# Kernel optimization log

Measured on AMD Instinct MI355X. Metric: run time of the kernel, lower is better.

## Reference

```python
import jax, jax.numpy as jnp
import numpy as np

N_NODES = 4096
N_HEADS = 8
NEG_SLOPE = 0.2  # PyG GATConv default leaky_relu slope


def _gat_single(h, src, dst, att_src, att_dst):
    # h: [N, H, C] projected node features; src/dst: [E] (self-loops included)
    a_s = (h * att_src).sum(-1)                      # [N, H]
    a_d = (h * att_dst).sum(-1)                      # [N, H]
    e = jax.nn.leaky_relu(a_s[src] + a_d[dst], NEG_SLOPE)   # [E, H]
    m = jax.ops.segment_max(e, dst, num_segments=N_NODES)   # [N, H]
    ex = jnp.exp(e - m[dst])                         # [E, H]
    denom = jax.ops.segment_sum(ex, dst, num_segments=N_NODES)
    alpha = ex / denom[dst]                          # [E, H] (self-loops => denom > 0)
    out = jax.ops.segment_sum(alpha[:, :, None] * h[src], dst, num_segments=N_NODES)
    return out                                       # [N, H, C]


def setup_inputs() -> dict:
    key = jax.random.key(0)
    ks = jax.random.split(key, 12)
    B, T, N, F = 4, 12, N_NODES, 8
    Hg, Hl = 64, 128
    inp = {
        "x": jax.random.normal(ks[0], (B, T, N, F), jnp.float32),
        "edge_index": jax.random.randint(ks[1], (2, 65536), 0, N, jnp.int64),
        "W_gat": jax.random.normal(ks[2], (F, Hg), jnp.float32) * 0.3,
        "att_src": jax.random.normal(ks[3], (N_HEADS, Hg // N_HEADS), jnp.float32) * 0.3,
        "att_dst": jax.random.normal(ks[4], (N_HEADS, Hg // N_HEADS), jnp.float32) * 0.3,
        "b_gat": jax.random.normal(ks[5], (Hg,), jnp.float32) * 0.1,
        "W_ih": jax.random.normal(ks[6], (4 * Hl, Hg * N), jnp.float32) * 0.002,
        "W_hh": jax.random.normal(ks[7], (4 * Hl, Hl), jnp.float32) * 0.05,
        "b_ih": jax.random.normal(ks[8], (4 * Hl,), jnp.float32) * 0.05,
        "b_hh": jax.random.normal(ks[9], (4 * Hl,), jnp.float32) * 0.05,
        "W_fc": jax.random.normal(ks[10], (Hl, N * F), jnp.float32) * 0.05,
        "b_fc": jax.random.normal(ks[11], (N * F,), jnp.float32) * 0.05,
    }
    return inp


def reference(x, edge_index, W_gat, att_src, att_dst, b_gat,
              W_ih, W_hh, b_ih, b_hh, W_fc, b_fc):
    B, T, N, F = x.shape
    H = N_HEADS
    C = W_gat.shape[1] // H
    Hl = W_hh.shape[1]

    # add self-loops (PyG GATConv default add_self_loops=True)
    loop = jnp.arange(N, dtype=edge_index.dtype)
    src = jnp.concatenate([edge_index[0], loop])
    dst = jnp.concatenate([edge_index[1], loop])

    # ---- GAT over all (batch, time) graphs at once ----
    h = (x.reshape(B * T, N, F) @ W_gat).reshape(B * T, N, H, C)
    gat = jax.vmap(_gat_single, in_axes=(0, None, None, None, None))(
        h, src, dst, att_src, att_dst)                # [BT, N, H, C]
    gat = gat.reshape(B * T, N, H * C) + b_gat
    gat = jax.nn.elu(gat)                             # dropout p=0 (eval) => identity
    seq = gat.reshape(B, T, N * H * C)

    # ---- LSTM (torch gate order: i, f, g, o) ----
    def step(carry, x_t):
        hprev, cprev = carry
        gates = x_t @ W_ih.T + b_ih + hprev @ W_hh.T + b_hh   # [B, 4Hl]
        i, f, g, o = jnp.split(gates, 4, axis=-1)
        c = jax.nn.sigmoid(f) * cprev + jax.nn.sigmoid(i) * jnp.tanh(g)
        hn = jax.nn.sigmoid(o) * jnp.tanh(c)
        return (hn, c), None

    h0 = jnp.zeros((B, Hl), x.dtype)
    (h_last, _), _ = jax.lax.scan(step, (h0, h0), seq.transpose(1, 0, 2))

    out = h_last @ W_fc + b_fc
    return out.reshape(B, N, F)
```

## Files before the change

### kernel.cpp

```cpp
#include <hip/hip_runtime.h>

#define NN 4096
#define NH 8
#define BTT 48
#define KG 262144
#define NJ 512
#define HLL 128
#define ERAW 65536
#define NKC 256
#define NG  24576

typedef __attribute__((ext_vector_type(8))) short bf16x8;
typedef __attribute__((ext_vector_type(4))) float f32x4;
typedef __attribute__((ext_vector_type(8))) unsigned short ushort8;

__device__ __forceinline__ unsigned short f2bf(float f) {
  unsigned int u = __float_as_uint(f);
  u += 0x7FFFu + ((u >> 16) & 1u);
  return (unsigned short)(u >> 16);
}
__device__ __forceinline__ float bf2f(unsigned short s) {
  return __uint_as_float(((unsigned int)s) << 16);
}

__global__ __launch_bounds__(256) void k_init(int* __restrict__ counts) {
  int t = blockIdx.x * 256 + threadIdx.x;
  counts[t] = 1;
}

__global__ __launch_bounds__(256) void k_hist(const int* __restrict__ ei, int* __restrict__ counts) {
  int e = blockIdx.x * 256 + threadIdx.x;
  atomicAdd(&counts[ei[ERAW + e]], 1);
}

__global__ __launch_bounds__(1024) void k_scan(const int* __restrict__ counts, int* __restrict__ offs,
                                               int* __restrict__ cursor, int* __restrict__ ssrc) {
  __shared__ int p[1024];
  int t = threadIdx.x;
  int i0 = t * 4;
  int c0 = counts[i0], c1 = counts[i0 + 1], c2 = counts[i0 + 2], c3 = counts[i0 + 3];
  int s = c0 + c1 + c2 + c3;
  p[t] = s;
  __syncthreads();
  for (int off = 1; off < 1024; off <<= 1) {
    int v = (t >= off) ? p[t - off] : 0;
    __syncthreads();
    p[t] += v;
    __syncthreads();
  }
  int base = p[t] - s;
  int o0 = base, o1 = o0 + c0, o2 = o1 + c1, o3 = o2 + c2;
  offs[i0] = o0; offs[i0 + 1] = o1; offs[i0 + 2] = o2; offs[i0 + 3] = o3;
  if (t == 1023) offs[NN] = o3 + c3;
  cursor[i0] = o0 + 1; cursor[i0 + 1] = o1 + 1; cursor[i0 + 2] = o2 + 1; cursor[i0 + 3] = o3 + 1;
  ssrc[o0] = i0; ssrc[o1] = i0 + 1; ssrc[o2] = i0 + 2; ssrc[o3] = i0 + 3;
}

__global__ __launch_bounds__(256) void k_scatter(const int* __restrict__ ei, int* __restrict__ cursor,
                                                 int* __restrict__ ssrc) {
  int e = blockIdx.x * 256 + threadIdx.x;
  int s = ei[e], d = ei[ERAW + e];
  int pos = atomicAdd(&cursor[d], 1);
  ssrc[pos] = s;
}

__global__ __launch_bounds__(256) void k_proj(const float* __restrict__ x, const float* __restrict__ Wg,
                                              const float* __restrict__ att_s, const float* __restrict__ att_d,
                                              unsigned short* __restrict__ h, float* __restrict__ a_s,
                                              float* __restrict__ a_d) {
  __shared__ float wgs[512];
  __shared__ float ats[64], atd[64];
  int tid = threadIdx.x;
  wgs[tid] = Wg[tid];
  wgs[256 + tid] = Wg[256 + tid];
  if (tid < 64) { ats[tid] = att_s[tid]; atd[tid] = att_d[tid]; }
  __syncthreads();
  int bt = blockIdx.x >> 7;
  int inner = blockIdx.x & 127;
  int hd = tid & 7, nl = tid >> 3;
  int n = inner * 32 + nl;
  const float* xr = x + ((size_t)(bt * NN + n)) * 8;
  float4 xa = *(const float4*)xr, xb2 = *(const float4*)(xr + 4);
  float xv[8] = {xa.x, xa.y, xa.z, xa.w, xb2.x, xb2.y, xb2.z, xb2.w};
  int hb = hd * 8;
  float hv[8];
#pragma unroll
  for (int c = 0; c < 8; ++c) {
    float acc = 0.f;
#pragma unroll
    for (int f = 0; f < 8; ++f) acc += xv[f] * wgs[f * 64 + hb + c];
    hv[c] = acc;
  }
  float as = 0.f, ad = 0.f;
#pragma unroll
  for (int c = 0; c < 8; ++c) { as += hv[c] * ats[hb + c]; ad += hv[c] * atd[hb + c]; }
  int aoff = bt * (NN * NH) + n * NH + hd;
  a_s[aoff] = as;
  a_d[aoff] = ad;
  ushort8 hr;
#pragma unroll
  for (int c = 0; c < 8; ++c) hr[c] = f2bf(hv[c]);
  *(ushort8*)(h + (size_t)bt * KG + (size_t)n * 64 + hb) = hr;
}

__global__ __launch_bounds__(256) void k_gat(const unsigned short* __restrict__ h, const float* __restrict__ a_s,
                                             const float* __restrict__ a_d, const int* __restrict__ offs,
                                             const int* __restrict__ ssrc, const float* __restrict__ b_gat,
                                             unsigned short* __restrict__ Xb) {
  int B = blockIdx.x;
  int xcd = B & 7;
  int slot = B >> 3;
  int btg = slot >> 7;
  int inner = slot & 127;
  int bt = btg * 8 + xcd;
  int tid = threadIdx.x;
  int hd = tid & 7, nl = tid >> 3;
  int n = inner * 32 + nl;
  const unsigned short* hbase = h + (size_t)bt * KG;
  const float* asb = a_s + bt * (NN * NH);
  float adn = a_d[bt * (NN * NH) + n * NH + hd];
  int beg = offs[n], end = offs[n + 1];
  float ssum = 0.f;
  float o[8];
#pragma unroll
  for (int c = 0; c < 8; ++c) o[c] = 0.f;
  for (int i = beg; i < end; ++i) {
    int s = ssrc[i];
    float e = asb[s * NH + hd] + adn;
    e = (e > 0.f) ? e : 0.2f * e;
    float p = __expf(e);
    ssum += p;
    ushort8 hvv = *(const ushort8*)(hbase + (size_t)s * 64 + hd * 8);
#pragma unroll
    for (int c = 0; c < 8; ++c) o[c] += p * bf2f(hvv[c]);
  }
  float inv = 1.f / ssum;
  ushort8 r;
#pragma unroll
  for (int c = 0; c < 8; ++c) {
    float v = o[c] * inv + b_gat[hd * 8 + c];
    v = (v > 0.f) ? v : (__expf(v) - 1.f);
    r[c] = f2bf(v);
  }
  *(ushort8*)(Xb + (size_t)bt * KG + (size_t)n * 64 + hd * 8) = r;
}

__global__ __launch_bounds__(256) void k_gemm(const unsigned short* __restrict__ Xb,
                                              const float* __restrict__ Wih, float* __restrict__ Gp) {
  int tid = threadIdx.x;
  int w = tid >> 6, lane = tid & 63;
  int lm = lane & 15, kg = lane >> 4;
  int b = blockIdx.x;
  int xcd = b & 7;
  int q = b >> 3;
  int kc = xcd * 32 + (q >> 2);
  int jb = q & 3;
  int j0 = jb * 128 + w * 32;
  size_t kbase = (size_t)kc * 1024 + kg * 8;

  const float* wr0 = Wih + (size_t)(j0 + lm) * KG + kbase;
  const float* wr1 = Wih + (size_t)(j0 + 16 + lm) * KG + kbase;
  const short* Xs = (const short*)Xb;
  const short* xr0 = Xs + (size_t)lm * KG + kbase;
  const short* xr1 = xr0 + (size_t)16 * KG;
  const short* xr2 = xr0 + (size_t)32 * KG;

  f32x4 acc[3][2];
#pragma unroll
  for (int mf = 0; mf < 3; ++mf)
#pragma unroll
    for (int jf = 0; jf < 2; ++jf) acc[mf][jf] = f32x4{0.f, 0.f, 0.f, 0.f};

  float4 wbuf[2][4];
  bf16x8 abuf[2][3];

  wbuf[0][0] = *(const float4*)(wr0);
  wbuf[0][1] = *(const float4*)(wr0 + 4);
  wbuf[0][2] = *(const float4*)(wr1);
  wbuf[0][3] = *(const float4*)(wr1 + 4);
  abuf[0][0] = *(const bf16x8*)(xr0);
  abuf[0][1] = *(const bf16x8*)(xr1);
  abuf[0][2] = *(const bf16x8*)(xr2);

#pragma unroll 2
  for (int t = 0; t < 32; ++t) {
    int cur = t & 1, nxt = cur ^ 1;
    if (t + 1 < 32) {
      int off = (t + 1) * 32;
      wbuf[nxt][0] = *(const float4*)(wr0 + off);
      wbuf[nxt][1] = *(const float4*)(wr0 + off + 4);
      wbuf[nxt][2] = *(const float4*)(wr1 + off);
      wbuf[nxt][3] = *(const float4*)(wr1 + off + 4);
      abuf[nxt][0] = *(const bf16x8*)(xr0 + off);
      abuf[nxt][1] = *(const bf16x8*)(xr1 + off);
      abuf[nxt][2] = *(const bf16x8*)(xr2 + off);
    }
#pragma unroll
    for (int jf = 0; jf < 2; ++jf) {
      float4 f0 = wbuf[cur][jf * 2], f1 = wbuf[cur][jf * 2 + 1];
      bf16x8 bb;
      bb[0] = (short)f2bf(f0.x); bb[1] = (short)f2bf(f0.y);
      bb[2] = (short)f2bf(f0.z); bb[3] = (short)f2bf(f0.w);
      bb[4] = (short)f2bf(f1.x); bb[5] = (short)f2bf(f1.y);
      bb[6] = (short)f2bf(f1.z); bb[7] = (short)f2bf(f1.w);
      acc[0][jf] = __builtin_amdgcn_mfma_f32_16x16x32_bf16(abuf[cur][0], bb, acc[0][jf], 0, 0, 0);
      acc[1][jf] = __builtin_amdgcn_mfma_f32_16x16x32_bf16(abuf[cur][1], bb, acc[1][jf], 0, 0, 0);
      acc[2][jf] = __builtin_amdgcn_mfma_f32_16x16x32_bf16(abuf[cur][2], bb, acc[2][jf], 0, 0, 0);
    }
  }

  float* gout = Gp + (size_t)kc * NG;
#pragma unroll
  for (int mf = 0; mf < 3; ++mf)
#pragma unroll
    for (int jf = 0; jf < 2; ++jf) {
      int j = j0 + jf * 16 + lm;
#pragma unroll
      for (int r = 0; r < 4; ++r) {
        int bt = mf * 16 + kg * 4 + r;
        gout[bt * NJ + j] = acc[mf][jf][r];
      }
    }
}

__global__ __launch_bounds__(256) void k_red1(const float* __restrict__ Gp, float* __restrict__ Gp2) {
  int idx = blockIdx.x * 256 + threadIdx.x;
  int seg = idx / NG;
  int gid = idx - seg * NG;
  const float* src = Gp + (size_t)seg * 32 * NG + gid;
  float acc = 0.f;
#pragma unroll 8
  for (int i = 0; i < 32; ++i) acc += src[(size_t)i * NG];
  Gp2[idx] = acc;
}

__global__ __launch_bounds__(512) void k_lstm(const float* __restrict__ Gp2, const float* __restrict__ Whh,
                                              const float* __restrict__ bih, const float* __restrict__ bhh,
                                              float* __restrict__ hlast) {
  __shared__ float hs[HLL];
  __shared__ float gs[NJ];
  int b = blockIdx.x, j = threadIdx.x;
  float bias = bih[j] + bhh[j];
  float w[HLL];
  const float* wr = Whh + (size_t)j * HLL;
#pragma unroll
  for (int k = 0; k < HLL; k += 4) {
    float4 v = *(const float4*)(wr + k);
    w[k] = v.x; w[k + 1] = v.y; w[k + 2] = v.z; w[k + 3] = v.w;
  }
  if (j < HLL) hs[j] = 0.f;
  float c = 0.f;
  __syncthreads();
  for (int t = 0; t < 12; ++t) {
    const float* gp = Gp2 + (size_t)(b * 12 + t) * NJ + j;
    float acc = bias;
#pragma unroll
    for (int s = 0; s < 8; ++s) acc += gp[(size_t)s * NG];
#pragma unroll
    for (int k = 0; k < HLL; ++k) acc += w[k] * hs[k];
    gs[j] = acc;
    __syncthreads();
    if (j < HLL) {
      float gi = gs[j], gf = gs[HLL + j], gg = gs[2 * HLL + j], go = gs[3 * HLL + j];
      float si = 1.f / (1.f + __expf(-gi));
      float sf = 1.f / (1.f + __expf(-gf));
      float so = 1.f / (1.f + __expf(-go));
      c = sf * c + si * tanhf(gg);
      hs[j] = so * tanhf(c);
    }
    __syncthreads();
  }
  if (j < HLL) hlast[b * HLL + j] = hs[j];
}

__global__ __launch_bounds__(256) void k_fc(const float* __restrict__ hlast, const float* __restrict__ Wfc,
                                            const float* __restrict__ bfc, float* __restrict__ out) {
  __shared__ float hl[NJ];
  int tid = threadIdx.x;
  hl[tid] = hlast[tid];
  hl[256 + tid] = hlast[256 + tid];
  __syncthreads();
  int n = blockIdx.x * 256 + tid;
  float a0 = 0.f, a1 = 0.f, a2 = 0.f, a3 = 0.f;
#pragma unroll 8
  for (int k = 0; k < HLL; ++k) {
    float wv = Wfc[(size_t)k * 32768 + n];
    a0 += hl[k] * wv;
    a1 += hl[HLL + k] * wv;
    a2 += hl[2 * HLL + k] * wv;
    a3 += hl[3 * HLL + k] * wv;
  }
  float bb = bfc[n];
  out[n] = a0 + bb;
  out[32768 + n] = a1 + bb;
  out[65536 + n] = a2 + bb;
  out[98304 + n] = a3 + bb;
}

extern "C" void kernel_launch(void* const* d_in, const int* in_sizes, int n_in,
                              void* d_out, int out_size, void* d_ws, size_t ws_size,
                              hipStream_t stream) {
  const float* x     = (const float*)d_in[0];
  const int*   ei    = (const int*)d_in[1];
  const float* Wg    = (const float*)d_in[2];
  const float* att_s = (const float*)d_in[3];
  const float* att_d = (const float*)d_in[4];
  const float* b_gat = (const float*)d_in[5];
  const float* Wih   = (const float*)d_in[6];
  const float* Whh   = (const float*)d_in[7];
  const float* bih   = (const float*)d_in[8];
  const float* bhh   = (const float*)d_in[9];
  const float* Wfc   = (const float*)d_in[10];
  const float* bfc   = (const float*)d_in[11];
  float* out = (float*)d_out;

  char* ws = (char*)d_ws;
  unsigned short* h  = (unsigned short*)(ws);
  float* a_s         = (float*)(ws + 25165824);
  float* a_d         = (float*)(ws + 31457280);
  unsigned short* Xb = (unsigned short*)(ws + 37748736);
  float* Gp          = (float*)(ws + 62914560);
  float* Gp2         = (float*)(ws + 88080384);
  float* hlast       = (float*)(ws + 88866816);
  int* counts        = (int*)(ws + 88868864);
  int* offs          = (int*)(ws + 88885248);
  int* cursor        = (int*)(ws + 88901644);
  int* ssrc          = (int*)(ws + 88918028);

  hipLaunchKernelGGL(k_init,    dim3(16),       dim3(256),  0, stream, counts);
  hipLaunchKernelGGL(k_hist,    dim3(256),      dim3(256),  0, stream, ei, counts);
  hipLaunchKernelGGL(k_scan,    dim3(1),        dim3(1024), 0, stream, counts, offs, cursor, ssrc);
  hipLaunchKernelGGL(k_scatter, dim3(256),      dim3(256),  0, stream, ei, cursor, ssrc);
  hipLaunchKernelGGL(k_proj,    dim3(48 * 128), dim3(256),  0, stream, x, Wg, att_s, att_d, h, a_s, a_d);
  hipLaunchKernelGGL(k_gat,     dim3(48 * 128), dim3(256),  0, stream, h, a_s, a_d, offs, ssrc, b_gat, Xb);
  hipLaunchKernelGGL(k_gemm,    dim3(1024),     dim3(256),  0, stream, Xb, Wih, Gp);
  hipLaunchKernelGGL(k_red1,    dim3(768),      dim3(256),  0, stream, Gp, Gp2);
  hipLaunchKernelGGL(k_lstm,    dim3(4),        dim3(512),  0, stream, Gp2, Whh, bih, bhh, hlast);
  hipLaunchKernelGGL(k_fc,      dim3(128),      dim3(256),  0, stream, hlast, Wfc, bfc, out);
}
```

Measured before the change: 320.1 us.

## Fuse whole pipeline into one cooperative persistent kernel with grid syncs

Replaces the ten separate launches with a single cooperative kernel of 512 blocks that runs the stages (histogram plus projection, scan, scatter, GAT, GEMM, reduction, LSTM, FC) separated by grid.sync. The GAT stage now processes two batch-time slices per edge walk, so the CSR index loads are shared across slices. The goal is to remove launch gaps and inter-kernel drain, at the cost of grid-barrier overhead and a fixed, smaller grid that may underfill stages such as the GEMM. The old multi-kernel path is kept as a fallback if the cooperative launch fails.

```diff
diff --git a/kernel.cpp b/kernel.cpp
--- a/kernel.cpp
+++ b/kernel.cpp
@@ -1,4 +1,7 @@
 #include <hip/hip_runtime.h>
+#include <hip/hip_cooperative_groups.h>
+
+namespace cg = cooperative_groups;
 
 #define NN 4096
 #define NH 8
@@ -23,16 +26,309 @@
   return __uint_as_float(((unsigned int)s) << 16);
 }
 
+__global__ __launch_bounds__(256, 2) void k_mega(
+    const float* __restrict__ x, const int* __restrict__ ei, const float* __restrict__ Wg,
+    const float* __restrict__ att_s, const float* __restrict__ att_d, const float* __restrict__ b_gat,
+    const float* __restrict__ Wih, const float* __restrict__ Whh, const float* __restrict__ bih,
+    const float* __restrict__ bhh, const float* __restrict__ Wfc, const float* __restrict__ bfc,
+    float* __restrict__ out, unsigned short* __restrict__ h, float* __restrict__ a_s,
+    float* __restrict__ a_d, unsigned short* __restrict__ Xb, float* __restrict__ Gp,
+    float* __restrict__ Gp2, float* __restrict__ hlast, int* __restrict__ counts,
+    int* __restrict__ offs, int* __restrict__ cursor, int* __restrict__ ssrc) {
+  cg::grid_group grid = cg::this_grid();
+  __shared__ float smem[768];
+  const int tid = threadIdx.x;
+  const int bid = blockIdx.x;
+  const int gid = bid * 256 + tid;
+
+  if (gid < ERAW) atomicAdd(&counts[ei[ERAW + gid]], 1);
+  smem[tid] = Wg[tid];
+  smem[256 + tid] = Wg[256 + tid];
+  if (tid < 64) { smem[512 + tid] = att_s[tid]; smem[576 + tid] = att_d[tid]; }
+  __syncthreads();
+  {
+    int hd = tid & 7, nl = tid >> 3, hb = hd * 8;
+    for (int iter = 0; iter < 12; ++iter) {
+      int vb = iter * 512 + bid;
+      int bt = vb >> 7, inner = vb & 127;
+      int n = inner * 32 + nl;
+      const float* xr = x + ((size_t)(bt * NN + n)) * 8;
+      float4 xa = *(const float4*)xr, xb2 = *(const float4*)(xr + 4);
+      float xv[8] = {xa.x, xa.y, xa.z, xa.w, xb2.x, xb2.y, xb2.z, xb2.w};
+      float hv[8];
+#pragma unroll
+      for (int c = 0; c < 8; ++c) {
+        float acc = 0.f;
+#pragma unroll
+        for (int f = 0; f < 8; ++f) acc += xv[f] * smem[f * 64 + hb + c];
+        hv[c] = acc;
+      }
+      float as = 0.f, ad = 0.f;
+#pragma unroll
+      for (int c = 0; c < 8; ++c) { as += hv[c] * smem[512 + hb + c]; ad += hv[c] * smem[576 + hb + c]; }
+      int aoff = bt * (NN * NH) + n * NH + hd;
+      a_s[aoff] = as;
+      a_d[aoff] = ad;
+      ushort8 hr;
+#pragma unroll
+      for (int c = 0; c < 8; ++c) hr[c] = f2bf(hv[c]);
+      *(ushort8*)(h + (size_t)bt * KG + (size_t)n * 64 + hb) = hr;
+    }
+  }
+  __threadfence();
+  grid.sync();
+
+  if (bid == 0) {
+    int* ip = (int*)smem;
+    int i0 = tid * 16;
+    int c[16];
+    int s = 0;
+#pragma unroll
+    for (int k = 0; k < 16; ++k) { c[k] = counts[i0 + k] + 1; s += c[k]; }
+    ip[tid] = s;
+    __syncthreads();
+    for (int off = 1; off < 256; off <<= 1) {
+      int v = (tid >= off) ? ip[tid - off] : 0;
+      __syncthreads();
+      ip[tid] += v;
+      __syncthreads();
+    }
+    int run = ip[tid] - s;
+#pragma unroll
+    for (int k = 0; k < 16; ++k) {
+      offs[i0 + k] = run;
+      cursor[i0 + k] = run + 1;
+      ssrc[run] = i0 + k;
+      run += c[k];
+    }
+    if (tid == 255) offs[NN] = run;
+  }
+  __threadfence();
+  grid.sync();
+
+  if (gid < ERAW) {
+    int s2 = ei[gid], d = ei[ERAW + gid];
+    int pos = atomicAdd(&cursor[d], 1);
+    ssrc[pos] = s2;
+  }
+  __threadfence();
+  grid.sync();
+
+  {
+    int hd = tid & 7, nl = tid >> 3, hb = hd * 8;
+    int xcd = bid & 7, q = bid >> 3;
+    float bg[8];
+#pragma unroll
+    for (int c = 0; c < 8; ++c) bg[c] = b_gat[hb + c];
+    for (int half = 0; half < 2; ++half) {
+      int n = (half * 64 + q) * 32 + nl;
+      int beg = offs[n], end = offs[n + 1];
+      for (int pr = 0; pr < 3; ++pr) {
+        int bt0 = (2 * pr) * 8 + xcd;
+        int bt1 = (2 * pr + 1) * 8 + xcd;
+        const unsigned short* hb0 = h + (size_t)bt0 * KG;
+        const unsigned short* hb1 = h + (size_t)bt1 * KG;
+        const float* as0 = a_s + bt0 * (NN * NH);
+        const float* as1 = a_s + bt1 * (NN * NH);
+        float ad0 = a_d[bt0 * (NN * NH) + n * NH + hd];
+        float ad1 = a_d[bt1 * (NN * NH) + n * NH + hd];
+        float ss0 = 0.f, ss1 = 0.f;
+        float o0[8], o1[8];
+#pragma unroll
+        for (int c = 0; c < 8; ++c) { o0[c] = 0.f; o1[c] = 0.f; }
+        for (int i = beg; i < end; ++i) {
+          int s = ssrc[i];
+          float e0 = as0[s * NH + hd] + ad0;
+          float e1 = as1[s * NH + hd] + ad1;
+          e0 = (e0 > 0.f) ? e0 : 0.2f * e0;
+          e1 = (e1 > 0.f) ? e1 : 0.2f * e1;
+          float p0 = __expf(e0), p1 = __expf(e1);
+          ss0 += p0; ss1 += p1;
+          ushort8 v0 = *(const ushort8*)(hb0 + (size_t)s * 64 + hb);
+          ushort8 v1 = *(const ushort8*)(hb1 + (size_t)s * 64 + hb);
+#pragma unroll
+          for (int c = 0; c < 8; ++c) { o0[c] += p0 * bf2f(v0[c]); o1[c] += p1 * bf2f(v1[c]); }
+        }
+        float i0 = 1.f / ss0, i1 = 1.f / ss1;
+        ushort8 r0, r1;
+#pragma unroll
+        for (int c = 0; c < 8; ++c) {
+          float u0 = o0[c] * i0 + bg[c];
+          float u1 = o1[c] * i1 + bg[c];
+          u0 = (u0 > 0.f) ? u0 : (__expf(u0) - 1.f);
+          u1 = (u1 > 0.f) ? u1 : (__expf(u1) - 1.f);
+          r0[c] = f2bf(u0); r1[c] = f2bf(u1);
+        }
+        *(ushort8*)(Xb + (size_t)bt0 * KG + (size_t)n * 64 + hb) = r0;
+        *(ushort8*)(Xb + (size_t)bt1 * KG + (size_t)n * 64 + hb) = r1;
+      }
+    }
+  }
+  __threadfence();
+  grid.sync();
+
+  {
+    int w = tid >> 6, lane = tid & 63;
+    int lm = lane & 15, kg = lane >> 4;
+    const short* Xs = (const short*)Xb;
+    for (int it = 0; it < 2; ++it) {
+      int vb = it * 512 + bid;
+      int jb = vb & 3;
+      int kc = vb >> 2;
+      int j0 = jb * 128 + w * 32;
+      size_t kbase = (size_t)kc * 1024 + kg * 8;
+
+      const float* wr0 = Wih + (size_t)(j0 + lm) * KG + kbase;
+      const float* wr1 = Wih + (size_t)(j0 + 16 + lm) * KG + kbase;
+      const short* xr0 = Xs + (size_t)lm * KG + kbase;
+      const short* xr1 = xr0 + (size_t)16 * KG;
+      const short* xr2 = xr0 + (size_t)32 * KG;
+
+      f32x4 acc[3][2];
+#pragma unroll
+      for (int mf = 0; mf < 3; ++mf)
+#pragma unroll
+        for (int jf = 0; jf < 2; ++jf) acc[mf][jf] = f32x4{0.f, 0.f, 0.f, 0.f};
+
+      float4 wbuf[2][4];
+      bf16x8 abuf[2][3];
+      wbuf[0][0] = *(const float4*)(wr0);
+      wbuf[0][1] = *(const float4*)(wr0 + 4);
+      wbuf[0][2] = *(const float4*)(wr1);
+      wbuf[0][3] = *(const float4*)(wr1 + 4);
+      abuf[0][0] = *(const bf16x8*)(xr0);
+      abuf[0][1] = *(const bf16x8*)(xr1);
+      abuf[0][2] = *(const bf16x8*)(xr2);
+
+#pragma unroll 2
+      for (int t = 0; t < 32; ++t) {
+        int cur = t & 1, nxt = cur ^ 1;
+        if (t + 1 < 32) {
+          int off = (t + 1) * 32;
+          wbuf[nxt][0] = *(const float4*)(wr0 + off);
+          wbuf[nxt][1] = *(const float4*)(wr0 + off + 4);
+          wbuf[nxt][2] = *(const float4*)(wr1 + off);
+          wbuf[nxt][3] = *(const float4*)(wr1 + off + 4);
+          abuf[nxt][0] = *(const bf16x8*)(xr0 + off);
+          abuf[nxt][1] = *(const bf16x8*)(xr1 + off);
+          abuf[nxt][2] = *(const bf16x8*)(xr2 + off);
+        }
+#pragma unroll
+        for (int jf = 0; jf < 2; ++jf) {
+          float4 f0 = wbuf[cur][jf * 2], f1 = wbuf[cur][jf * 2 + 1];
+          bf16x8 bb;
+          bb[0] = (short)f2bf(f0.x); bb[1] = (short)f2bf(f0.y);
+          bb[2] = (short)f2bf(f0.z); bb[3] = (short)f2bf(f0.w);
+          bb[4] = (short)f2bf(f1.x); bb[5] = (short)f2bf(f1.y);
+          bb[6] = (short)f2bf(f1.z); bb[7] = (short)f2bf(f1.w);
+          acc[0][jf] = __builtin_amdgcn_mfma_f32_16x16x32_bf16(abuf[cur][0], bb, acc[0][jf], 0, 0, 0);
+          acc[1][jf] = __builtin_amdgcn_mfma_f32_16x16x32_bf16(abuf[cur][1], bb, acc[1][jf], 0, 0, 0);
+          acc[2][jf] = __builtin_amdgcn_mfma_f32_16x16x32_bf16(abuf[cur][2], bb, acc[2][jf], 0, 0, 0);
+        }
+      }
+
+      float* gout = Gp + (size_t)kc * NG;
+#pragma unroll
+      for (int mf = 0; mf < 3; ++mf)
+#pragma unroll
+        for (int jf = 0; jf < 2; ++jf) {
+          int j = j0 + jf * 16 + lm;
+#pragma unroll
+          for (int r = 0; r < 4; ++r) {
+            int bt = mf * 16 + kg * 4 + r;
+            gout[bt * NJ + j] = acc[mf][jf][r];
+          }
+        }
+    }
+  }
+  __threadfence();
+  grid.sync();
+
+  for (int idx = gid; idx < 8 * NG; idx += 512 * 256) {
+    int seg = idx / NG;
+    int g2 = idx - seg * NG;
+    const float* src = Gp + (size_t)seg * 32 * NG + g2;
+    float acc = 0.f;
+#pragma unroll 8
+    for (int i = 0; i < 32; ++i) acc += src[(size_t)i * NG];
+    Gp2[idx] = acc;
+  }
+  __threadfence();
+  grid.sync();
+
+  if (bid < 4) {
+    float* hs = smem;
+    float* gs = smem + 128;
+    int b = bid;
+    int j0 = tid, j1 = tid + 256;
+    float bias0 = bih[j0] + bhh[j0];
+    float bias1 = bih[j1] + bhh[j1];
+    if (tid < 128) hs[tid] = 0.f;
+    float cc = 0.f;
+    __syncthreads();
+    const float4* w0 = (const float4*)(Whh + (size_t)j0 * HLL);
+    const float4* w1 = (const float4*)(Whh + (size_t)j1 * HLL);
+    for (int t = 0; t < 12; ++t) {
+      const float* gp = Gp2 + (size_t)(b * 12 + t) * NJ;
+      float acc0 = bias0, acc1 = bias1;
+#pragma unroll
+      for (int s = 0; s < 8; ++s) { acc0 += gp[s * NG + j0]; acc1 += gp[s * NG + j1]; }
+#pragma unroll 8
+      for (int k = 0; k < 32; ++k) {
+        float4 wa = w0[k], wb = w1[k];
+        int kb = k * 4;
+        acc0 += wa.x * hs[kb] + wa.y * hs[kb + 1] + wa.z * hs[kb + 2] + wa.w * hs[kb + 3];
+        acc1 += wb.x * hs[kb] + wb.y * hs[kb + 1] + wb.z * hs[kb + 2] + wb.w * hs[kb + 3];
+      }
+      gs[j0] = acc0;
+      gs[j1] = acc1;
+      __syncthreads();
+      if (tid < 128) {
+        float gi = gs[tid], gf = gs[128 + tid], gg = gs[256 + tid], go = gs[384 + tid];
+        float si = 1.f / (1.f + __expf(-gi));
+        float sf = 1.f / (1.f + __expf(-gf));
+        float so = 1.f / (1.f + __expf(-go));
+        cc = sf * cc + si * tanhf(gg);
+        hs[tid] = so * tanhf(cc);
+      }
+      __syncthreads();
+    }
+    if (tid < 128) hlast[b * HLL + tid] = hs[tid];
+  }
+  __threadfence();
+  grid.sync();
+
+  if (bid < 128) {
+    float* hl = smem;
+    hl[tid] = hlast[tid];
+    hl[256 + tid] = hlast[256 + tid];
+    __syncthreads();
+    int n = bid * 256 + tid;
+    float a0 = 0.f, a1 = 0.f, a2 = 0.f, a3 = 0.f;
+#pragma unroll 8
+    for (int k = 0; k < HLL; ++k) {
+      float wv = Wfc[(size_t)k * 32768 + n];
+      a0 += hl[k] * wv;
+      a1 += hl[HLL + k] * wv;
+      a2 += hl[2 * HLL + k] * wv;
+      a3 += hl[3 * HLL + k] * wv;
+    }
+    float bb = bfc[n];
+    out[n] = a0 + bb;
+    out[32768 + n] = a1 + bb;
+    out[65536 + n] = a2 + bb;
+    out[98304 + n] = a3 + bb;
+  }
+}
+
 __global__ __launch_bounds__(256) void k_init(int* __restrict__ counts) {
   int t = blockIdx.x * 256 + threadIdx.x;
   counts[t] = 1;
 }
-
 __global__ __launch_bounds__(256) void k_hist(const int* __restrict__ ei, int* __restrict__ counts) {
   int e = blockIdx.x * 256 + threadIdx.x;
   atomicAdd(&counts[ei[ERAW + e]], 1);
 }
-
 __global__ __launch_bounds__(1024) void k_scan(const int* __restrict__ counts, int* __restrict__ offs,
                                                int* __restrict__ cursor, int* __restrict__ ssrc) {
   __shared__ int p[1024];
@@ -55,7 +351,6 @@
   cursor[i0] = o0 + 1; cursor[i0 + 1] = o1 + 1; cursor[i0 + 2] = o2 + 1; cursor[i0 + 3] = o3 + 1;
   ssrc[o0] = i0; ssrc[o1] = i0 + 1; ssrc[o2] = i0 + 2; ssrc[o3] = i0 + 3;
 }
-
 __global__ __launch_bounds__(256) void k_scatter(const int* __restrict__ ei, int* __restrict__ cursor,
                                                  int* __restrict__ ssrc) {
   int e = blockIdx.x * 256 + threadIdx.x;
@@ -63,7 +358,6 @@
   int pos = atomicAdd(&cursor[d], 1);
   ssrc[pos] = s;
 }
-
 __global__ __launch_bounds__(256) void k_proj(const float* __restrict__ x, const float* __restrict__ Wg,
                                               const float* __restrict__ att_s, const float* __restrict__ att_d,
                                               unsigned short* __restrict__ h, float* __restrict__ a_s,
@@ -102,7 +396,6 @@
   for (int c = 0; c < 8; ++c) hr[c] = f2bf(hv[c]);
   *(ushort8*)(h + (size_t)bt * KG + (size_t)n * 64 + hb) = hr;
 }
-
 __global__ __launch_bounds__(256) void k_gat(const unsigned short* __restrict__ h, const float* __restrict__ a_s,
                                              const float* __restrict__ a_d, const int* __restrict__ offs,
                                              const int* __restrict__ ssrc, const float* __restrict__ b_gat,
@@ -144,36 +437,28 @@
   }
   *(ushort8*)(Xb + (size_t)bt * KG + (size_t)n * 64 + hd * 8) = r;
 }
-
 __global__ __launch_bounds__(256) void k_gemm(const unsigned short* __restrict__ Xb,
                                               const float* __restrict__ Wih, float* __restrict__ Gp) {
   int tid = threadIdx.x;
   int w = tid >> 6, lane = tid & 63;
   int lm = lane & 15, kg = lane >> 4;
-  int b = blockIdx.x;
-  int xcd = b & 7;
-  int q = b >> 3;
-  int kc = xcd * 32 + (q >> 2);
-  int jb = q & 3;
+  int jb = blockIdx.x & 3;
+  int kc = blockIdx.x >> 2;
   int j0 = jb * 128 + w * 32;
   size_t kbase = (size_t)kc * 1024 + kg * 8;
-
   const float* wr0 = Wih + (size_t)(j0 + lm) * KG + kbase;
   const float* wr1 = Wih + (size_t)(j0 + 16 + lm) * KG + kbase;
   const short* Xs = (const short*)Xb;
   const short* xr0 = Xs + (size_t)lm * KG + kbase;
   const short* xr1 = xr0 + (size_t)16 * KG;
   const short* xr2 = xr0 + (size_t)32 * KG;
-
   f32x4 acc[3][2];
 #pragma unroll
   for (int mf = 0; mf < 3; ++mf)
 #pragma unroll
     for (int jf = 0; jf < 2; ++jf) acc[mf][jf] = f32x4{0.f, 0.f, 0.f, 0.f};
-
   float4 wbuf[2][4];
   bf16x8 abuf[2][3];
-
   wbuf[0][0] = *(const float4*)(wr0);
   wbuf[0][1] = *(const float4*)(wr0 + 4);
   wbuf[0][2] = *(const float4*)(wr1);
@@ -181,7 +466,6 @@
   abuf[0][0] = *(const bf16x8*)(xr0);
   abuf[0][1] = *(const bf16x8*)(xr1);
   abuf[0][2] = *(const bf16x8*)(xr2);
-
 #pragma unroll 2
   for (int t = 0; t < 32; ++t) {
     int cur = t & 1, nxt = cur ^ 1;
@@ -208,7 +492,6 @@
       acc[2][jf] = __builtin_amdgcn_mfma_f32_16x16x32_bf16(abuf[cur][2], bb, acc[2][jf], 0, 0, 0);
     }
   }
-
   float* gout = Gp + (size_t)kc * NG;
 #pragma unroll
   for (int mf = 0; mf < 3; ++mf)
@@ -222,7 +505,6 @@
       }
     }
 }
-
 __global__ __launch_bounds__(256) void k_red1(const float* __restrict__ Gp, float* __restrict__ Gp2) {
   int idx = blockIdx.x * 256 + threadIdx.x;
   int seg = idx / NG;
@@ -233,7 +515,6 @@
   for (int i = 0; i < 32; ++i) acc += src[(size_t)i * NG];
   Gp2[idx] = acc;
 }
-
 __global__ __launch_bounds__(512) void k_lstm(const float* __restrict__ Gp2, const float* __restrict__ Whh,
                                               const float* __restrict__ bih, const float* __restrict__ bhh,
                                               float* __restrict__ hlast) {
@@ -272,7 +553,6 @@
   }
   if (j < HLL) hlast[b * HLL + j] = hs[j];
 }
-
 __global__ __launch_bounds__(256) void k_fc(const float* __restrict__ hlast, const float* __restrict__ Wfc,
                                             const float* __restrict__ bfc, float* __restrict__ out) {
   __shared__ float hl[NJ];
@@ -324,17 +604,28 @@
   float* hlast       = (float*)(ws + 88866816);
   int* counts        = (int*)(ws + 88868864);
   int* offs          = (int*)(ws + 88885248);
-  int* cursor        = (int*)(ws + 88901644);
-  int* ssrc          = (int*)(ws + 88918028);
-
-  hipLaunchKernelGGL(k_init,    dim3(16),       dim3(256),  0, stream, counts);
-  hipLaunchKernelGGL(k_hist,    dim3(256),      dim3(256),  0, stream, ei, counts);
-  hipLaunchKernelGGL(k_scan,    dim3(1),        dim3(1024), 0, stream, counts, offs, cursor, ssrc);
-  hipLaunchKernelGGL(k_scatter, dim3(256),      dim3(256),  0, stream, ei, cursor, ssrc);
-  hipLaunchKernelGGL(k_proj,    dim3(48 * 128), dim3(256),  0, stream, x, Wg, att_s, att_d, h, a_s, a_d);
-  hipLaunchKernelGGL(k_gat,     dim3(48 * 128), dim3(256),  0, stream, h, a_s, a_d, offs, ssrc, b_gat, Xb);
-  hipLaunchKernelGGL(k_gemm,    dim3(1024),     dim3(256),  0, stream, Xb, Wih, Gp);
-  hipLaunchKernelGGL(k_red1,    dim3(768),      dim3(256),  0, stream, Gp, Gp2);
-  hipLaunchKernelGGL(k_lstm,    dim3(4),        dim3(512),  0, stream, Gp2, Whh, bih, bhh, hlast);
-  hipLaunchKernelGGL(k_fc,      dim3(128),      dim3(256),  0, stream, hlast, Wfc, bfc, out);
-}
+  int* cursor        = (int*)(ws + 88901648);
+  int* ssrc          = (int*)(ws + 88918032);
+
+  hipMemsetAsync(counts, 0, NN * sizeof(int), stream);
+
+  void* args[] = {
+      (void*)&x, (void*)&ei, (void*)&Wg, (void*)&att_s, (void*)&att_d, (void*)&b_gat,
+      (void*)&Wih, (void*)&Whh, (void*)&bih, (void*)&bhh, (void*)&Wfc, (void*)&bfc,
+      (void*)&out, (void*)&h, (void*)&a_s, (void*)&a_d, (void*)&Xb, (void*)&Gp,
+      (void*)&Gp2, (void*)&hlast, (void*)&counts, (void*)&offs, (void*)&cursor, (void*)&ssrc};
+  hipError_t err = hipLaunchCooperativeKernel((void*)k_mega, dim3(512), dim3(256), args, 0, stream);
+
+  if (err != hipSuccess) {
+    hipLaunchKernelGGL(k_init,    dim3(16),       dim3(256),  0, stream, counts);
+    hipLaunchKernelGGL(k_hist,    dim3(256),      dim3(256),  0, stream, ei, counts);
+    hipLaunchKernelGGL(k_scan,    dim3(1),        dim3(1024), 0, stream, counts, offs, cursor, ssrc);
+    hipLaunchKernelGGL(k_scatter, dim3(256),      dim3(256),  0, stream, ei, cursor, ssrc);
+    hipLaunchKernelGGL(k_proj,    dim3(48 * 128), dim3(256),  0, stream, x, Wg, att_s, att_d, h, a_s, a_d);
+    hipLaunchKernelGGL(k_gat,     dim3(48 * 128), dim3(256),  0, stream, h, a_s, a_d, offs, ssrc, b_gat, Xb);
+    hipLaunchKernelGGL(k_gemm,    dim3(1024),     dim3(256),  0, stream, Xb, Wih, Gp);
+    hipLaunchKernelGGL(k_red1,    dim3(768),      dim3(256),  0, stream, Gp, Gp2);
+    hipLaunchKernelGGL(k_lstm,    dim3(4),        dim3(512),  0, stream, Gp2, Whh, bih, bhh, hlast);
+    hipLaunchKernelGGL(k_fc,      dim3(128),      dim3(256),  0, stream, hlast, Wfc, bfc, out);
+  }
+}
```

New measurement: 1.089 ms. 3.4x slower.

## Replace CSR build with fixed-capacity per-node buckets, add nontemporal weight loads

Applied to the files above, without the earlier changes.

Removes the count, histogram and single-block scan kernels. Edges and self-loops are now scattered directly into fixed 64-slot buckets per destination node, with the atomic cursor serving as the degree. The GEMM streams W_ih with nontemporal loads and drops the XCD-aware block remapping. The bucket scheme assumes in-degree never exceeds 64, which is a data-dependent risk: random edges give a mean in-degree of about 17, so overflow is unlikely but not ruled out.

```diff
diff --git a/kernel.cpp b/kernel.cpp
--- a/kernel.cpp
+++ b/kernel.cpp
@@ -9,6 +9,7 @@
 #define ERAW 65536
 #define NKC 256
 #define NG  24576
+#define CAP 64
 
 typedef __attribute__((ext_vector_type(8))) short bf16x8;
 typedef __attribute__((ext_vector_type(4))) float f32x4;
@@ -22,46 +23,23 @@
 __device__ __forceinline__ float bf2f(unsigned short s) {
   return __uint_as_float(((unsigned int)s) << 16);
 }
-
-__global__ __launch_bounds__(256) void k_init(int* __restrict__ counts) {
-  int t = blockIdx.x * 256 + threadIdx.x;
-  counts[t] = 1;
-}
-
-__global__ __launch_bounds__(256) void k_hist(const int* __restrict__ ei, int* __restrict__ counts) {
-  int e = blockIdx.x * 256 + threadIdx.x;
-  atomicAdd(&counts[ei[ERAW + e]], 1);
-}
-
-__global__ __launch_bounds__(1024) void k_scan(const int* __restrict__ counts, int* __restrict__ offs,
-                                               int* __restrict__ cursor, int* __restrict__ ssrc) {
-  __shared__ int p[1024];
-  int t = threadIdx.x;
-  int i0 = t * 4;
-  int c0 = counts[i0], c1 = counts[i0 + 1], c2 = counts[i0 + 2], c3 = counts[i0 + 3];
-  int s = c0 + c1 + c2 + c3;
-  p[t] = s;
-  __syncthreads();
-  for (int off = 1; off < 1024; off <<= 1) {
-    int v = (t >= off) ? p[t - off] : 0;
-    __syncthreads();
-    p[t] += v;
-    __syncthreads();
-  }
-  int base = p[t] - s;
-  int o0 = base, o1 = o0 + c0, o2 = o1 + c1, o3 = o2 + c2;
-  offs[i0] = o0; offs[i0 + 1] = o1; offs[i0 + 2] = o2; offs[i0 + 3] = o3;
-  if (t == 1023) offs[NN] = o3 + c3;
-  cursor[i0] = o0 + 1; cursor[i0 + 1] = o1 + 1; cursor[i0 + 2] = o2 + 1; cursor[i0 + 3] = o3 + 1;
-  ssrc[o0] = i0; ssrc[o1] = i0 + 1; ssrc[o2] = i0 + 2; ssrc[o3] = i0 + 3;
+__device__ __forceinline__ float4 nt_load4(const float* p) {
+  f32x4 v = __builtin_nontemporal_load((const f32x4*)p);
+  return float4{v[0], v[1], v[2], v[3]};
 }
 
 __global__ __launch_bounds__(256) void k_scatter(const int* __restrict__ ei, int* __restrict__ cursor,
                                                  int* __restrict__ ssrc) {
-  int e = blockIdx.x * 256 + threadIdx.x;
-  int s = ei[e], d = ei[ERAW + e];
-  int pos = atomicAdd(&cursor[d], 1);
-  ssrc[pos] = s;
+  int t = blockIdx.x * 256 + threadIdx.x;
+  if (t < ERAW) {
+    int s = ei[t], d = ei[ERAW + t];
+    int pos = atomicAdd(&cursor[d], 1);
+    ssrc[(d << 6) + pos] = s;
+  } else {
+    int n = t - ERAW;
+    int pos = atomicAdd(&cursor[n], 1);
+    ssrc[(n << 6) + pos] = n;
+  }
 }
 
 __global__ __launch_bounds__(256) void k_proj(const float* __restrict__ x, const float* __restrict__ Wg,
@@ -104,7 +82,7 @@
 }
 
 __global__ __launch_bounds__(256) void k_gat(const unsigned short* __restrict__ h, const float* __restrict__ a_s,
-                                             const float* __restrict__ a_d, const int* __restrict__ offs,
+                                             const float* __restrict__ a_d, const int* __restrict__ cursor,
                                              const int* __restrict__ ssrc, const float* __restrict__ b_gat,
                                              unsigned short* __restrict__ Xb) {
   int B = blockIdx.x;
@@ -119,13 +97,14 @@
   const unsigned short* hbase = h + (size_t)bt * KG;
   const float* asb = a_s + bt * (NN * NH);
   float adn = a_d[bt * (NN * NH) + n * NH + hd];
-  int beg = offs[n], end = offs[n + 1];
+  int deg = cursor[n];
+  const int* bucket = ssrc + (n << 6);
   float ssum = 0.f;
   float o[8];
 #pragma unroll
   for (int c = 0; c < 8; ++c) o[c] = 0.f;
-  for (int i = beg; i < end; ++i) {
-    int s = ssrc[i];
+  for (int i = 0; i < deg; ++i) {
+    int s = bucket[i];
     float e = asb[s * NH + hd] + adn;
     e = (e > 0.f) ? e : 0.2f * e;
     float p = __expf(e);
@@ -150,11 +129,8 @@
   int tid = threadIdx.x;
   int w = tid >> 6, lane = tid & 63;
   int lm = lane & 15, kg = lane >> 4;
-  int b = blockIdx.x;
-  int xcd = b & 7;
-  int q = b >> 3;
-  int kc = xcd * 32 + (q >> 2);
-  int jb = q & 3;
+  int jb = blockIdx.x & 3;
+  int kc = blockIdx.x >> 2;
   int j0 = jb * 128 + w * 32;
   size_t kbase = (size_t)kc * 1024 + kg * 8;
 
@@ -174,10 +150,10 @@
   float4 wbuf[2][4];
   bf16x8 abuf[2][3];
 
-  wbuf[0][0] = *(const float4*)(wr0);
-  wbuf[0][1] = *(const float4*)(wr0 + 4);
-  wbuf[0][2] = *(const float4*)(wr1);
-  wbuf[0][3] = *(const float4*)(wr1 + 4);
+  wbuf[0][0] = nt_load4(wr0);
+  wbuf[0][1] = nt_load4(wr0 + 4);
+  wbuf[0][2] = nt_load4(wr1);
+  wbuf[0][3] = nt_load4(wr1 + 4);
   abuf[0][0] = *(const bf16x8*)(xr0);
   abuf[0][1] = *(const bf16x8*)(xr1);
   abuf[0][2] = *(const bf16x8*)(xr2);
@@ -187,10 +163,10 @@
     int cur = t & 1, nxt = cur ^ 1;
     if (t + 1 < 32) {
       int off = (t + 1) * 32;
-      wbuf[nxt][0] = *(const float4*)(wr0 + off);
-      wbuf[nxt][1] = *(const float4*)(wr0 + off + 4);
-      wbuf[nxt][2] = *(const float4*)(wr1 + off);
-      wbuf[nxt][3] = *(const float4*)(wr1 + off + 4);
+      wbuf[nxt][0] = nt_load4(wr0 + off);
+      wbuf[nxt][1] = nt_load4(wr0 + off + 4);
+      wbuf[nxt][2] = nt_load4(wr1 + off);
+      wbuf[nxt][3] = nt_load4(wr1 + off + 4);
       abuf[nxt][0] = *(const bf16x8*)(xr0 + off);
       abuf[nxt][1] = *(const bf16x8*)(xr1 + off);
       abuf[nxt][2] = *(const bf16x8*)(xr2 + off);
@@ -320,21 +296,17 @@
   float* a_d         = (float*)(ws + 31457280);
   unsigned short* Xb = (unsigned short*)(ws + 37748736);
   float* Gp          = (float*)(ws + 62914560);
+  int* ssrc          = (int*)(ws + 87031808);
   float* Gp2         = (float*)(ws + 88080384);
   float* hlast       = (float*)(ws + 88866816);
-  int* counts        = (int*)(ws + 88868864);
-  int* offs          = (int*)(ws + 88885248);
-  int* cursor        = (int*)(ws + 88901644);
-  int* ssrc          = (int*)(ws + 88918028);
-
-  hipLaunchKernelGGL(k_init,    dim3(16),       dim3(256),  0, stream, counts);
-  hipLaunchKernelGGL(k_hist,    dim3(256),      dim3(256),  0, stream, ei, counts);
-  hipLaunchKernelGGL(k_scan,    dim3(1),        dim3(1024), 0, stream, counts, offs, cursor, ssrc);
-  hipLaunchKernelGGL(k_scatter, dim3(256),      dim3(256),  0, stream, ei, cursor, ssrc);
-  hipLaunchKernelGGL(k_proj,    dim3(48 * 128), dim3(256),  0, stream, x, Wg, att_s, att_d, h, a_s, a_d);
-  hipLaunchKernelGGL(k_gat,     dim3(48 * 128), dim3(256),  0, stream, h, a_s, a_d, offs, ssrc, b_gat, Xb);
-  hipLaunchKernelGGL(k_gemm,    dim3(1024),     dim3(256),  0, stream, Xb, Wih, Gp);
-  hipLaunchKernelGGL(k_red1,    dim3(768),      dim3(256),  0, stream, Gp, Gp2);
-  hipLaunchKernelGGL(k_lstm,    dim3(4),        dim3(512),  0, stream, Gp2, Whh, bih, bhh, hlast);
-  hipLaunchKernelGGL(k_fc,      dim3(128),      dim3(256),  0, stream, hlast, Wfc, bfc, out);
-}
+  int* cursor        = (int*)(ws + 88868864);
+
+  hipMemsetAsync(cursor, 0, NN * sizeof(int), stream);
+  hipLaunchKernelGGL(k_scatter, dim3(272),      dim3(256), 0, stream, ei, cursor, ssrc);
+  hipLaunchKernelGGL(k_proj,    dim3(48 * 128), dim3(256), 0, stream, x, Wg, att_s, att_d, h, a_s, a_d);
+  hipLaunchKernelGGL(k_gat,     dim3(48 * 128), dim3(256), 0, stream, h, a_s, a_d, cursor, ssrc, b_gat, Xb);
+  hipLaunchKernelGGL(k_gemm,    dim3(1024),     dim3(256), 0, stream, Xb, Wih, Gp);
+  hipLaunchKernelGGL(k_red1,    dim3(768),      dim3(256), 0, stream, Gp, Gp2);
+  hipLaunchKernelGGL(k_lstm,    dim3(4),        dim3(512), 0, stream, Gp2, Whh, bih, bhh, hlast);
+  hipLaunchKernelGGL(k_fc,      dim3(128),      dim3(256), 0, stream, hlast, Wfc, bfc, out);
+}
```

New measurement: 312.5 us. 1.02x faster.
